# Optimization experiments

Hardware: AMD Instinct MI355X
Metric: run time of the kernel (lower is better)

## Reference

```python
import jax, jax.numpy as jnp
import numpy as np

HIDDEN = 1024
EMB = HIDDEN // 2          # embedding_dim = hidden_dim // 2
NUM_OPS = 8
BATCH = 16384


def setup_inputs() -> dict:
    key = jax.random.key(0)
    ks = jax.random.split(key, 8)
    x = jax.random.normal(ks[0], (BATCH, HIDDEN), dtype=jnp.float32)
    sampled_ops = jax.random.randint(ks[1], (BATCH,), 0, NUM_OPS, dtype=jnp.int32)
    op_emb = jax.random.normal(ks[2], (NUM_OPS, EMB), dtype=jnp.float32) * 0.02
    # per-expert 2-layer MLP params (Linear stored as [in, out] for x @ W)
    s1 = 1.0 / np.sqrt(HIDDEN + EMB)
    s2 = 1.0 / np.sqrt(HIDDEN)
    W1 = jax.random.uniform(ks[3], (NUM_OPS, HIDDEN + EMB, HIDDEN), jnp.float32, -s1, s1)
    b1 = jax.random.uniform(ks[4], (NUM_OPS, HIDDEN), jnp.float32, -s1, s1)
    W2 = jax.random.uniform(ks[5], (NUM_OPS, HIDDEN, HIDDEN), jnp.float32, -s2, s2)
    b2 = jax.random.uniform(ks[6], (NUM_OPS, HIDDEN), jnp.float32, -s2, s2)
    return {"x": x, "sampled_ops": sampled_ops, "op_emb": op_emb,
            "W1": W1, "b1": b1, "W2": W2, "b2": b2}


def reference(x, sampled_ops, op_emb, W1, b1, W2, b2):
    # gather per-token operator embedding and augment input
    emb = jnp.take(op_emb, sampled_ops, axis=0)            # [B, EMB]
    x_aug = jnp.concatenate([x, emb], axis=-1)             # [B, H+EMB]
    num_ops = W1.shape[0]
    out = jnp.zeros_like(x)
    # loop over the small fixed expert set; mask-combine per token
    for o in range(num_ops):
        h = jax.nn.relu(x_aug @ W1[o] + b1[o])             # [B, H]
        y = jax.nn.relu(h @ W2[o] + b2[o])                 # [B, H]
        mask = (sampled_ops == o)[:, None]
        out = out + jnp.where(mask, y, 0.0)
    return out
```

## Files before the change

### kernel.cpp

```cpp
#include <hip/hip_runtime.h>
#include <hip/hip_bf16.h>

#define BATCH 16384
#define HID   1024
#define EMBD  512
#define NOPS  8
#define MAXT  136
#define CNTS  16

typedef __attribute__((ext_vector_type(8))) short bf16x8;
typedef __attribute__((ext_vector_type(4))) float f32x4;

__device__ __forceinline__ unsigned short f2bf(float f) {
  unsigned int u = __float_as_uint(f);
  u += 0x7FFF + ((u >> 16) & 1);
  return (unsigned short)(u >> 16);
}

__device__ __forceinline__ unsigned int pk2(float a, float b) {
  __hip_bfloat162 t = __float22bfloat162_rn(make_float2(a, b));
  return *(unsigned int*)(&t);
}

__device__ __forceinline__ void lds_load16(void* lds, const void* g) {
  __builtin_amdgcn_global_load_lds(
      (const __attribute__((address_space(1))) unsigned int*)g,
      (__attribute__((address_space(3))) unsigned int*)lds, 16, 0, 0);
}

__device__ __forceinline__ void decode_bid(int bid, int& g, int& nx) {
  g = 17 * (bid & 7) + (bid >> 6);
  nx = (bid >> 3) & 7;
}

__device__ __forceinline__ int decode_tile(const int* __restrict__ cnt,
                                           int g, int& rs, int& ce_cnt) {
  int e = -1, at = 0;
  rs = 0; ce_cnt = 0;
#pragma unroll
  for (int o = 0; o < NOPS; ++o) {
    int c = cnt[o * CNTS];
    int t = (c + 127) >> 7;
    if (e < 0 && g < at + t) { e = o; rs = (g - at) * 128; ce_cnt = c; }
    at += t;
  }
  return e;
}

__device__ __forceinline__ void w_prep_tile(const float* __restrict__ W,
                                            short* __restrict__ Wp,
                                            int ks, int nx, int tid) {
  int n = tid & 127, kh = tid >> 7;
  const float* src = W + (size_t)(ks * 32 + kh * 16) * 1024 + nx * 128 + n;
  float v[16];
#pragma unroll
  for (int kk = 0; kk < 16; ++kk) v[kk] = src[(size_t)kk * 1024];
  uint4 a, b;
  a.x = pk2(v[0], v[1]);  a.y = pk2(v[2], v[3]);
  a.z = pk2(v[4], v[5]);  a.w = pk2(v[6], v[7]);
  b.x = pk2(v[8], v[9]);  b.y = pk2(v[10], v[11]);
  b.z = pk2(v[12], v[13]); b.w = pk2(v[14], v[15]);
  uint4* dst = (uint4*)Wp;
  dst[(2 * kh) * 128 + n]     = a;
  dst[(2 * kh + 1) * 128 + n] = b;
}

__global__ void bucket_ce_k(const int* __restrict__ ops, int* __restrict__ cnt,
                            int* __restrict__ idx, const float* __restrict__ W1,
                            const float* __restrict__ emb,
                            const float* __restrict__ b1, float* __restrict__ ce,
                            short* __restrict__ W1p, const float* __restrict__ x,
                            unsigned int* __restrict__ xb) {
  int bid = blockIdx.x;
  int tid = threadIdx.x;
  if (bid >= 2240) {
    size_t i = ((size_t)(bid - 2240) * 256 + tid) * 16;
    const float4* src = (const float4*)(x + i);
    float4 f0 = src[0], f1 = src[1], f2v = src[2], f3 = src[3];
    uint4 p0 = make_uint4(pk2(f0.x, f0.y), pk2(f0.z, f0.w),
                          pk2(f1.x, f1.y), pk2(f1.z, f1.w));
    uint4 p1 = make_uint4(pk2(f2v.x, f2v.y), pk2(f2v.z, f2v.w),
                          pk2(f3.x, f3.y), pk2(f3.z, f3.w));
    uint4* dst = (uint4*)(xb + i / 2);
    dst[0] = p0;
    dst[1] = p1;
    return;
  }
  if (bid >= 192) {
    int b = bid - 192;
    int e = b / 256; int rr = b % 256; int nx = rr / 32, ks = rr % 32;
    w_prep_tile(W1 + (size_t)e * 1536 * 1024,
                W1p + ((size_t)(e * 8 + nx) * 32 + ks) * 4096, ks, nx, tid);
    return;
  }
  if (bid >= 64) {
    int cb = bid - 64;
    int e = cb >> 4, kp = cb & 15;
    int n = tid * 4;
    const float* Wc = W1 + (size_t)e * 1536 * 1024 + (size_t)(1024 + kp * 32) * 1024 + n;
    const float* ee = emb + e * EMBD + kp * 32;
    float4 a = make_float4(0.f, 0.f, 0.f, 0.f);
#pragma unroll
    for (int kk = 0; kk < 32; ++kk) {
      float s = ee[kk];
      float4 r = *(const float4*)(Wc + (size_t)kk * 1024);
      a.x += s * r.x; a.y += s * r.y; a.z += s * r.z; a.w += s * r.w;
    }
    if (kp == 0) {
      float4 b = *(const float4*)(b1 + e * HID + n);
      a.x += b.x; a.y += b.y; a.z += b.z; a.w += b.w;
    }
    float* d = ce + e * HID + n;
    atomicAdd(d + 0, a.x); atomicAdd(d + 1, a.y);
    atomicAdd(d + 2, a.z); atomicAdd(d + 3, a.w);
    return;
  }
  __shared__ int wcnt[4][NOPS];
  __shared__ int wbase[4][NOPS];
  int lane = tid & 63, w = tid >> 6;
  int t = bid * 256 + tid;
  int op = ops[t];
  unsigned long long msave = 0;
#pragma unroll
  for (int o = 0; o < NOPS; ++o) {
    unsigned long long mm = __ballot(op == o);
    if (op == o) msave = mm;
    if (lane == o) wcnt[w][o] = __popcll(mm);
  }
  __syncthreads();
  if (tid < NOPS) {
    int c0 = wcnt[0][tid], c1 = wcnt[1][tid], c2 = wcnt[2][tid], c3 = wcnt[3][tid];
    int base = atomicAdd(&cnt[tid * CNTS], c0 + c1 + c2 + c3);
    wbase[0][tid] = base;
    wbase[1][tid] = base + c0;
    wbase[2][tid] = base + c0 + c1;
    wbase[3][tid] = base + c0 + c1 + c2;
  }
  __syncthreads();
  int pre = __popcll(msave & ((1ull << lane) - 1ull));
  idx[op * BATCH + wbase[w][op] + pre] = t;
}

__global__ __launch_bounds__(256) void gemm1_w2_k(
    const unsigned int* __restrict__ xb, const int* __restrict__ idx,
    const float* __restrict__ ce, const short* __restrict__ W1p,
    unsigned short* __restrict__ hp, const int* __restrict__ cnt,
    const float* __restrict__ W2, short* __restrict__ W2p) {
  int bid = blockIdx.x;
  int tid = threadIdx.x;
  if (bid >= 8 * MAXT) {
    int b = bid - 8 * MAXT;
    int e = b / 256; int rr = b % 256; int nx = rr / 32, ks = rr % 32;
    w_prep_tile(W2 + (size_t)e * 1024 * 1024,
                W2p + ((size_t)(e * 8 + nx) * 32 + ks) * 4096, ks, nx, tid);
    return;
  }
  int g, nx;
  decode_bid(bid, g, nx);
  int rs, ce_cnt;
  int e = decode_tile(cnt, g, rs, ce_cnt);
  if (e < 0) return;

  __shared__ __align__(16) char smem[32768];
  char* s0 = smem;
  char* s1 = smem + 16384;

  int lane = tid & 63, w = tid >> 6;
  int wm = w >> 1, wn = w & 1;
  int fr = lane & 15, fq = lane >> 4;

  int p0 = rs + lane, p1 = rs + 64 + lane;
  int t0 = (p0 < ce_cnt) ? idx[e * BATCH + p0] : 0;
  int t1 = (p1 < ce_cnt) ? idx[e * BATCH + p1] : 0;
  const char* a0 = (const char*)xb + (size_t)t0 * 2048 + w * 16;
  const char* a1 = (const char*)xb + (size_t)t1 * 2048 + w * 16;
  const char* Bsrc = (const char*)W1p + (size_t)(e * 8 + nx) * 32 * 8192;

  lds_load16(s0 + w * 2048,         a0);
  lds_load16(s0 + w * 2048 + 1024,  a1);
  lds_load16(s0 + 8192 + w * 1024,  Bsrc + w * 1024 + lane * 16);
  lds_load16(s0 + 12288 + w * 1024, Bsrc + 4096 + w * 1024 + lane * 16);
  asm volatile("s_waitcnt vmcnt(0)" ::: "memory");
  __builtin_amdgcn_s_barrier();

  f32x4 acc[4][4] = {};
  int fo = (fq * 128 + wm * 64 + fr) * 8;
  int bo = (fq * 128 + wn * 64 + fr) * 8;

#define G1_STEP(CURB, NXTB, KS)                                               \
  {                                                                           \
    if ((KS) < 31) {                                                          \
      const char* bs_ = Bsrc + ((KS) + 1) * 8192;                             \
      lds_load16((NXTB) + w * 2048,         a0 + ((KS) + 1) * 64);            \
      lds_load16((NXTB) + w * 2048 + 1024,  a1 + ((KS) + 1) * 64);            \
      lds_load16((NXTB) + 8192 + w * 1024,  bs_ + w * 1024 + lane * 16);      \
      lds_load16((NXTB) + 12288 + w * 1024, bs_ + 4096 + w * 1024 + lane * 16); \
    }                                                                         \
    const short* lA_ = (const short*)(CURB);                                  \
    const short* lB_ = (const short*)((CURB) + 8192);                         \
    bf16x8 af[4], bfr[4];                                                     \
    _Pragma("unroll")                                                         \
    for (int i = 0; i < 4; ++i) af[i] = *(const bf16x8*)&lA_[fo + i * 128];   \
    _Pragma("unroll")                                                         \
    for (int j = 0; j < 4; ++j) bfr[j] = *(const bf16x8*)&lB_[bo + j * 128];  \
    _Pragma("unroll")                                                         \
    for (int i = 0; i < 4; ++i)                                               \
      _Pragma("unroll")                                                       \
      for (int j = 0; j < 4; ++j)                                             \
        acc[i][j] = __builtin_amdgcn_mfma_f32_16x16x32_bf16(af[i], bfr[j],    \
                                                            acc[i][j], 0, 0, 0); \
    asm volatile("s_waitcnt vmcnt(0)" ::: "memory");                          \
    __builtin_amdgcn_s_barrier();                                             \
  }

  for (int ks = 0; ks < 32; ks += 2) {
    G1_STEP(s0, s1, ks);
    G1_STEP(s1, s0, ks + 1);
  }
#undef G1_STEP

  float bias[4];
#pragma unroll
  for (int j = 0; j < 4; ++j)
    bias[j] = ce[e * HID + nx * 128 + wn * 64 + j * 16 + fr];

  int lr = lane >> 2;
#pragma unroll
  for (int i = 0; i < 4; ++i) {
    __syncthreads();
#pragma unroll
    for (int j = 0; j < 4; ++j)
#pragma unroll
      for (int rg = 0; rg < 4; ++rg) {
        float v = acc[i][j][rg] + bias[j];
        v = v > 0.f ? v : 0.f;
        int row16 = fq * 4 + rg;
        int off = w * 2048 + row16 * 128 + (j * 16 + fr) * 2;
        off ^= (row16 & 1) << 6;
        *(unsigned short*)(smem + off) = f2bf(v);
      }
    __syncthreads();
    int R = wm * 64 + i * 16 + lr;
#pragma unroll
    for (int s = 0; s < 2; ++s) {
      int ch = (lane & 3) + s * 4;
      int off = w * 2048 + lr * 128 + ch * 16;
      off ^= (lr & 1) << 6;
      uint4 val = *(const uint4*)(smem + off);
      int ks2 = nx * 4 + wn * 2 + (ch >> 2);
      int kq = ch & 3;
      *(uint4*)(hp + (((size_t)(g * 32 + ks2) * 4 + kq) * 128 + R) * 8) = val;
    }
  }
}

__global__ __launch_bounds__(256) void gemm2_k(
    const unsigned short* __restrict__ hp, const float* __restrict__ b2,
    const short* __restrict__ W2p, float* __restrict__ out,
    const int* __restrict__ idx, const int* __restrict__ cnt) {
  int g, nx;
  decode_bid(blockIdx.x, g, nx);
  int rs, ce_cnt;
  int e = decode_tile(cnt, g, rs, ce_cnt);
  if (e < 0) return;

  __shared__ __align__(16) char smem[32768];
  __shared__ int toks[128];
  char* s0 = smem;
  char* s1 = smem + 16384;

  int tid = threadIdx.x, lane = tid & 63, w = tid >> 6;
  int wm = w >> 1, wn = w & 1;
  int fr = lane & 15, fq = lane >> 4;

  if (tid < 128) {
    int p = rs + tid;
    toks[tid] = (p < ce_cnt) ? idx[e * BATCH + p] : 0;
  }

  const char* Asrc = (const char*)hp + (size_t)g * 32 * 8192;
  const char* Bsrc = (const char*)W2p + (size_t)(e * 8 + nx) * 32 * 8192;

  lds_load16(s0 + w * 1024,         Asrc + w * 1024 + lane * 16);
  lds_load16(s0 + 4096 + w * 1024,  Asrc + 4096 + w * 1024 + lane * 16);
  lds_load16(s0 + 8192 + w * 1024,  Bsrc + w * 1024 + lane * 16);
  lds_load16(s0 + 12288 + w * 1024, Bsrc + 4096 + w * 1024 + lane * 16);
  asm volatile("s_waitcnt vmcnt(0)" ::: "memory");
  __builtin_amdgcn_s_barrier();

  f32x4 acc[4][4] = {};
  int fo = (fq * 128 + wm * 64 + fr) * 8;
  int bo = (fq * 128 + wn * 64 + fr) * 8;

#define G2_STEP(CURB, NXTB, KS)                                               \
  {                                                                           \
    if ((KS) < 31) {                                                          \
      const char* as_ = Asrc + ((KS) + 1) * 8192;                             \
      const char* bs_ = Bsrc + ((KS) + 1) * 8192;                             \
      lds_load16((NXTB) + w * 1024,         as_ + w * 1024 + lane * 16);      \
      lds_load16((NXTB) + 4096 + w * 1024,  as_ + 4096 + w * 1024 + lane * 16); \
      lds_load16((NXTB) + 8192 + w * 1024,  bs_ + w * 1024 + lane * 16);      \
      lds_load16((NXTB) + 12288 + w * 1024, bs_ + 4096 + w * 1024 + lane * 16); \
    }                                                                         \
    const short* lA_ = (const short*)(CURB);                                  \
    const short* lB_ = (const short*)((CURB) + 8192);                         \
    bf16x8 af[4], bfr[4];                                                     \
    _Pragma("unroll")                                                         \
    for (int i = 0; i < 4; ++i) af[i] = *(const bf16x8*)&lA_[fo + i * 128];   \
    _Pragma("unroll")                                                         \
    for (int j = 0; j < 4; ++j) bfr[j] = *(const bf16x8*)&lB_[bo + j * 128];  \
    _Pragma("unroll")                                                         \
    for (int i = 0; i < 4; ++i)                                               \
      _Pragma("unroll")                                                       \
      for (int j = 0; j < 4; ++j)                                             \
        acc[i][j] = __builtin_amdgcn_mfma_f32_16x16x32_bf16(af[i], bfr[j],    \
                                                            acc[i][j], 0, 0, 0); \
    asm volatile("s_waitcnt vmcnt(0)" ::: "memory");                          \
    __builtin_amdgcn_s_barrier();                                             \
  }

  for (int ks = 0; ks < 32; ks += 2) {
    G2_STEP(s0, s1, ks);
    G2_STEP(s1, s0, ks + 1);
  }
#undef G2_STEP

  float bias[4];
#pragma unroll
  for (int j = 0; j < 4; ++j)
    bias[j] = b2[e * HID + nx * 128 + wn * 64 + j * 16 + fr];

  int lr = lane >> 2;
#pragma unroll
  for (int i = 0; i < 4; ++i) {
    __syncthreads();
#pragma unroll
    for (int j = 0; j < 4; ++j)
#pragma unroll
      for (int rg = 0; rg < 4; ++rg) {
        float v = acc[i][j][rg] + bias[j];
        int row16 = fq * 4 + rg;
        int off = w * 4096 + row16 * 256 + (j * 16 + fr) * 4;
        off ^= (row16 & 1) << 6;
        *(float*)(smem + off) = v > 0.f ? v : 0.f;
      }
    __syncthreads();
    int R = wm * 64 + i * 16 + lr;
    if (R < ce_cnt - rs) {
      float* orow = out + (size_t)toks[R] * HID + nx * 128 + wn * 64;
#pragma unroll
      for (int s = 0; s < 4; ++s) {
        int ch = (lane & 3) + s * 4;
        int off = w * 4096 + lr * 256 + ch * 16;
        off ^= (lr & 1) << 6;
        *(float4*)(orow + ch * 4) = *(const float4*)(smem + off);
      }
    }
  }
}


extern "C" void kernel_launch(void* const* d_in, const int* in_sizes, int n_in,
                              void* d_out, int out_size, void* d_ws, size_t ws_size,
                              hipStream_t stream) {
  const float* x   = (const float*)d_in[0];
  const int*   ops = (const int*)d_in[1];
  const float* emb = (const float*)d_in[2];
  const float* W1  = (const float*)d_in[3];
  const float* b1  = (const float*)d_in[4];
  const float* W2  = (const float*)d_in[5];
  const float* b2  = (const float*)d_in[6];
  float* out = (float*)d_out;

  char* ws = (char*)d_ws;
  int* cnt  = (int*)(ws + 0);
  float* ce = (float*)(ws + 512);
  int* idx  = (int*)(ws + 36864);
  short* W1p = (short*)(ws + 561152);
  short* W2p = (short*)(ws + 17338368);
  unsigned short* hp = (unsigned short*)(ws + 34115584);
  unsigned int* xb = (unsigned int*)(ws + 69767168);

  hipMemsetAsync(ws, 0, 33280, stream);
  bucket_ce_k<<<2240 + 4096, 256, 0, stream>>>(ops, cnt, idx, W1, emb, b1, ce, W1p, x, xb);
  gemm1_w2_k<<<8 * MAXT + 2048, 256, 0, stream>>>(xb, idx, ce, W1p, hp, cnt, W2, W2p);
  gemm2_k<<<8 * MAXT, 256, 0, stream>>>(hp, b2, W2p, out, idx, cnt);
}
```

Before: 304.2 us.

## Use three-stage LDS pipeline with partial vmcnt waits in both expert GEMMs

Both grouped GEMM kernels move from double-buffered LDS staging, which waited on all outstanding loads every k-step, to a triple-buffered ring. Each step keeps one stage of global-to-LDS loads in flight by waiting with vmcnt(4) rather than vmcnt(0). Launch bounds now request 3 blocks per CU and LDS per block grows to 48KB. The aim is to hide global load latency behind MFMA work, at the cost of more LDS per block, which may limit occupancy.

```diff
diff --git a/kernel.cpp b/kernel.cpp
--- a/kernel.cpp
+++ b/kernel.cpp
@@ -10,6 +10,15 @@
 
 typedef __attribute__((ext_vector_type(8))) short bf16x8;
 typedef __attribute__((ext_vector_type(4))) float f32x4;
+
+#define VMWAIT(N) asm volatile("s_waitcnt vmcnt(" #N ")" ::: "memory")
+#define BARRIER_FENCED()                      \
+  do {                                        \
+    asm volatile("" ::: "memory");            \
+    __builtin_amdgcn_s_barrier();             \
+    asm volatile("" ::: "memory");            \
+    __builtin_amdgcn_sched_barrier(0);        \
+  } while (0)
 
 __device__ __forceinline__ unsigned short f2bf(float f) {
   unsigned int u = __float_as_uint(f);
@@ -141,7 +150,7 @@
   idx[op * BATCH + wbase[w][op] + pre] = t;
 }
 
-__global__ __launch_bounds__(256) void gemm1_w2_k(
+__global__ __launch_bounds__(256, 3) void gemm1_w2_k(
     const unsigned int* __restrict__ xb, const int* __restrict__ idx,
     const float* __restrict__ ce, const short* __restrict__ W1p,
     unsigned short* __restrict__ hp, const int* __restrict__ cnt,
@@ -161,9 +170,10 @@
   int e = decode_tile(cnt, g, rs, ce_cnt);
   if (e < 0) return;
 
-  __shared__ __align__(16) char smem[32768];
+  __shared__ __align__(16) char smem[49152];
   char* s0 = smem;
   char* s1 = smem + 16384;
+  char* s2 = smem + 32768;
 
   int lane = tid & 63, w = tid >> 6;
   int wm = w >> 1, wn = w & 1;
@@ -172,32 +182,25 @@
   int p0 = rs + lane, p1 = rs + 64 + lane;
   int t0 = (p0 < ce_cnt) ? idx[e * BATCH + p0] : 0;
   int t1 = (p1 < ce_cnt) ? idx[e * BATCH + p1] : 0;
-  const char* a0 = (const char*)xb + (size_t)t0 * 2048 + w * 16;
-  const char* a1 = (const char*)xb + (size_t)t1 * 2048 + w * 16;
-  const char* Bsrc = (const char*)W1p + (size_t)(e * 8 + nx) * 32 * 8192;
-
-  lds_load16(s0 + w * 2048,         a0);
-  lds_load16(s0 + w * 2048 + 1024,  a1);
-  lds_load16(s0 + 8192 + w * 1024,  Bsrc + w * 1024 + lane * 16);
-  lds_load16(s0 + 12288 + w * 1024, Bsrc + 4096 + w * 1024 + lane * 16);
-  asm volatile("s_waitcnt vmcnt(0)" ::: "memory");
-  __builtin_amdgcn_s_barrier();
-
-  f32x4 acc[4][4] = {};
-  int fo = (fq * 128 + wm * 64 + fr) * 8;
-  int bo = (fq * 128 + wn * 64 + fr) * 8;
-
-#define G1_STEP(CURB, NXTB, KS)                                               \
-  {                                                                           \
-    if ((KS) < 31) {                                                          \
-      const char* bs_ = Bsrc + ((KS) + 1) * 8192;                             \
-      lds_load16((NXTB) + w * 2048,         a0 + ((KS) + 1) * 64);            \
-      lds_load16((NXTB) + w * 2048 + 1024,  a1 + ((KS) + 1) * 64);            \
-      lds_load16((NXTB) + 8192 + w * 1024,  bs_ + w * 1024 + lane * 16);      \
-      lds_load16((NXTB) + 12288 + w * 1024, bs_ + 4096 + w * 1024 + lane * 16); \
-    }                                                                         \
-    const short* lA_ = (const short*)(CURB);                                  \
-    const short* lB_ = (const short*)((CURB) + 8192);                         \
+  const char* pa0 = (const char*)xb + (size_t)t0 * 2048 + w * 16;
+  const char* pa1 = (const char*)xb + (size_t)t1 * 2048 + w * 16;
+  const char* pb0 = (const char*)W1p + (size_t)(e * 8 + nx) * 32 * 8192
+                    + w * 1024 + lane * 16;
+  const char* pb1 = pb0 + 4096;
+
+#define G1_STAGE(NB)                                                          \
+  {                                                                           \
+    lds_load16((NB) + w * 2048,         pa0);                                 \
+    lds_load16((NB) + w * 2048 + 1024,  pa1);                                 \
+    lds_load16((NB) + 8192 + w * 1024,  pb0);                                 \
+    lds_load16((NB) + 12288 + w * 1024, pb1);                                 \
+    pa0 += 64; pa1 += 64; pb0 += 8192; pb1 += 8192;                           \
+  }
+
+#define G1_COMP(CB)                                                           \
+  {                                                                           \
+    const short* lA_ = (const short*)(CB);                                    \
+    const short* lB_ = (const short*)((CB) + 8192);                           \
     bf16x8 af[4], bfr[4];                                                     \
     _Pragma("unroll")                                                         \
     for (int i = 0; i < 4; ++i) af[i] = *(const bf16x8*)&lA_[fo + i * 128];   \
@@ -209,15 +212,38 @@
       for (int j = 0; j < 4; ++j)                                             \
         acc[i][j] = __builtin_amdgcn_mfma_f32_16x16x32_bf16(af[i], bfr[j],    \
                                                             acc[i][j], 0, 0, 0); \
-    asm volatile("s_waitcnt vmcnt(0)" ::: "memory");                          \
-    __builtin_amdgcn_s_barrier();                                             \
-  }
-
-  for (int ks = 0; ks < 32; ks += 2) {
-    G1_STEP(s0, s1, ks);
-    G1_STEP(s1, s0, ks + 1);
-  }
+  }
+
+#define G1_STEP(CB, NB)                                                       \
+  {                                                                           \
+    G1_STAGE(NB);                                                             \
+    G1_COMP(CB);                                                              \
+    VMWAIT(4);                                                                \
+    BARRIER_FENCED();                                                         \
+  }
+
+  G1_STAGE(s0);
+  G1_STAGE(s1);
+  VMWAIT(4);
+  BARRIER_FENCED();
+
+  f32x4 acc[4][4] = {};
+  int fo = (fq * 128 + wm * 64 + fr) * 8;
+  int bo = (fq * 128 + wn * 64 + fr) * 8;
+
+  for (int it = 0; it < 10; ++it) {
+    G1_STEP(s0, s2);
+    G1_STEP(s1, s0);
+    G1_STEP(s2, s1);
+  }
+  G1_COMP(s0);
+  VMWAIT(0);
+  BARRIER_FENCED();
+  G1_COMP(s1);
+
 #undef G1_STEP
+#undef G1_COMP
+#undef G1_STAGE
 
   float bias[4];
 #pragma unroll
@@ -254,7 +280,7 @@
   }
 }
 
-__global__ __launch_bounds__(256) void gemm2_k(
+__global__ __launch_bounds__(256, 3) void gemm2_k(
     const unsigned short* __restrict__ hp, const float* __restrict__ b2,
     const short* __restrict__ W2p, float* __restrict__ out,
     const int* __restrict__ idx, const int* __restrict__ cnt) {
@@ -264,10 +290,11 @@
   int e = decode_tile(cnt, g, rs, ce_cnt);
   if (e < 0) return;
 
-  __shared__ __align__(16) char smem[32768];
+  __shared__ __align__(16) char smem[49152];
   __shared__ int toks[128];
   char* s0 = smem;
   char* s1 = smem + 16384;
+  char* s2 = smem + 32768;
 
   int tid = threadIdx.x, lane = tid & 63, w = tid >> 6;
   int wm = w >> 1, wn = w & 1;
@@ -280,30 +307,24 @@
 
   const char* Asrc = (const char*)hp + (size_t)g * 32 * 8192;
   const char* Bsrc = (const char*)W2p + (size_t)(e * 8 + nx) * 32 * 8192;
-
-  lds_load16(s0 + w * 1024,         Asrc + w * 1024 + lane * 16);
-  lds_load16(s0 + 4096 + w * 1024,  Asrc + 4096 + w * 1024 + lane * 16);
-  lds_load16(s0 + 8192 + w * 1024,  Bsrc + w * 1024 + lane * 16);
-  lds_load16(s0 + 12288 + w * 1024, Bsrc + 4096 + w * 1024 + lane * 16);
-  asm volatile("s_waitcnt vmcnt(0)" ::: "memory");
-  __builtin_amdgcn_s_barrier();
-
-  f32x4 acc[4][4] = {};
-  int fo = (fq * 128 + wm * 64 + fr) * 8;
-  int bo = (fq * 128 + wn * 64 + fr) * 8;
-
-#define G2_STEP(CURB, NXTB, KS)                                               \
-  {                                                                           \
-    if ((KS) < 31) {                                                          \
-      const char* as_ = Asrc + ((KS) + 1) * 8192;                             \
-      const char* bs_ = Bsrc + ((KS) + 1) * 8192;                             \
-      lds_load16((NXTB) + w * 1024,         as_ + w * 1024 + lane * 16);      \
-      lds_load16((NXTB) + 4096 + w * 1024,  as_ + 4096 + w * 1024 + lane * 16); \
-      lds_load16((NXTB) + 8192 + w * 1024,  bs_ + w * 1024 + lane * 16);      \
-      lds_load16((NXTB) + 12288 + w * 1024, bs_ + 4096 + w * 1024 + lane * 16); \
-    }                                                                         \
-    const short* lA_ = (const short*)(CURB);                                  \
-    const short* lB_ = (const short*)((CURB) + 8192);                         \
+  const char* pA0 = Asrc + w * 1024 + lane * 16;
+  const char* pA1 = pA0 + 4096;
+  const char* pB0 = Bsrc + w * 1024 + lane * 16;
+  const char* pB1 = pB0 + 4096;
+
+#define G2_STAGE(NB)                                                          \
+  {                                                                           \
+    lds_load16((NB) + w * 1024,         pA0);                                 \
+    lds_load16((NB) + 4096 + w * 1024,  pA1);                                 \
+    lds_load16((NB) + 8192 + w * 1024,  pB0);                                 \
+    lds_load16((NB) + 12288 + w * 1024, pB1);                                 \
+    pA0 += 8192; pA1 += 8192; pB0 += 8192; pB1 += 8192;                       \
+  }
+
+#define G2_COMP(CB)                                                           \
+  {                                                                           \
+    const short* lA_ = (const short*)(CB);                                    \
+    const short* lB_ = (const short*)((CB) + 8192);                           \
     bf16x8 af[4], bfr[4];                                                     \
     _Pragma("unroll")                                                         \
     for (int i = 0; i < 4; ++i) af[i] = *(const bf16x8*)&lA_[fo + i * 128];   \
@@ -315,15 +336,38 @@
       for (int j = 0; j < 4; ++j)                                             \
         acc[i][j] = __builtin_amdgcn_mfma_f32_16x16x32_bf16(af[i], bfr[j],    \
                                                             acc[i][j], 0, 0, 0); \
-    asm volatile("s_waitcnt vmcnt(0)" ::: "memory");                          \
-    __builtin_amdgcn_s_barrier();                                             \
-  }
-
-  for (int ks = 0; ks < 32; ks += 2) {
-    G2_STEP(s0, s1, ks);
-    G2_STEP(s1, s0, ks + 1);
-  }
+  }
+
+#define G2_STEP(CB, NB)                                                       \
+  {                                                                           \
+    G2_STAGE(NB);                                                             \
+    G2_COMP(CB);                                                              \
+    VMWAIT(4);                                                                \
+    BARRIER_FENCED();                                                         \
+  }
+
+  G2_STAGE(s0);
+  G2_STAGE(s1);
+  VMWAIT(4);
+  BARRIER_FENCED();
+
+  f32x4 acc[4][4] = {};
+  int fo = (fq * 128 + wm * 64 + fr) * 8;
+  int bo = (fq * 128 + wn * 64 + fr) * 8;
+
+  for (int it = 0; it < 10; ++it) {
+    G2_STEP(s0, s2);
+    G2_STEP(s1, s0);
+    G2_STEP(s2, s1);
+  }
+  G2_COMP(s0);
+  VMWAIT(0);
+  BARRIER_FENCED();
+  G2_COMP(s1);
+
 #undef G2_STEP
+#undef G2_COMP
+#undef G2_STAGE
 
   float bias[4];
 #pragma unroll
```

Measured after the change: 295.2 us. -2.9%, faster.
